# Performance work log

Measured on AMD Instinct MI355X. Metric: run time of the kernel, lower is better.

## Reference

```python
import jax, jax.numpy as jnp
import numpy as np

EPS = 1e-6


def _ln(x, gamma, beta):
    # torch LayerNorm variant here: uses unbiased std (ddof=1) and eps added to std
    mean = jnp.mean(x, axis=-1, keepdims=True)
    std = jnp.std(x, axis=-1, keepdims=True, ddof=1)
    return gamma * (x - mean) / (std + EPS) + beta


def setup_inputs() -> dict:
    key = jax.random.key(0)
    ks = jax.random.split(key, 5)
    B, In, H = 8192, 1024, 1024
    x = jax.random.normal(ks[0], (B, In), dtype=jnp.float32)
    h = jax.random.normal(ks[1], (B, H), dtype=jnp.float32)
    c = jax.random.normal(ks[2], (B, H), dtype=jnp.float32)
    w_ih = jax.random.normal(ks[3], (4 * H, In), dtype=jnp.float32) * (1.0 / np.sqrt(In))
    b_ih = jnp.zeros((4 * H,), dtype=jnp.float32)
    w_hh = jax.random.normal(ks[4], (4 * H, H), dtype=jnp.float32) * (1.0 / np.sqrt(H))
    gamma_ifgo = jnp.ones((4, H), dtype=jnp.float32)
    beta_ifgo = jnp.zeros((4, H), dtype=jnp.float32)
    gamma_c = jnp.ones((H,), dtype=jnp.float32)
    beta_c = jnp.zeros((H,), dtype=jnp.float32)
    return {"x": x, "h": h, "c": c, "w_ih": w_ih, "b_ih": b_ih, "w_hh": w_hh,
            "gamma_ifgo": gamma_ifgo, "beta_ifgo": beta_ifgo,
            "gamma_c": gamma_c, "beta_c": beta_c}


def reference(x, h, c, w_ih, b_ih, w_hh, gamma_ifgo, beta_ifgo, gamma_c, beta_c):
    B = x.shape[0]
    H = c.shape[1]
    # two GEMMs: [B,4H]
    v = jnp.einsum('bi,ki->bk', x, w_ih) + b_ih + jnp.einsum('bh,kh->bk', h, w_hh)
    gates = v.reshape(B, 4, H)  # stacked i, f, g, o (chunk order == stack order)
    gates = _ln(gates, gamma_ifgo, beta_ifgo)  # ParallelLayerNorm over last dim
    i, f, g, o = gates[:, 0], gates[:, 1], gates[:, 2], gates[:, 3]
    f = f + 1.0
    new_c = c * jax.nn.sigmoid(f) + jax.nn.sigmoid(i) * jnp.tanh(g)
    new_c = _ln(new_c, gamma_c, beta_c)
    new_h = jnp.tanh(new_c) * jax.nn.sigmoid(o)
    return new_h, new_c
```

## Files before the change

### kernel.cpp

```cpp
#include <hip/hip_runtime.h>
#include <hip/hip_bf16.h>
#include <cstdint>

typedef __bf16 bf16x8 __attribute__((ext_vector_type(8)));
typedef float  f32x4  __attribute__((ext_vector_type(4)));

#define BDIM 8192
#define KDIM 2048
#define NDIM 4096
#define HDIM 1024
#define LN_EPS 1e-6f
#define NT    (KDIM / 64)

__global__ __launch_bounds__(256) void cvt_concat_kernel(
    const float* __restrict__ p0, const float* __restrict__ p1,
    __bf16* __restrict__ dst, long total)
{
    long e = ((long)blockIdx.x * blockDim.x + threadIdx.x) * 8;
    if (e >= total) return;
    long row = e >> 11;
    long kk  = e & 2047;
    const float* src = (kk < 1024) ? (p0 + row * 1024 + kk)
                                   : (p1 + row * 1024 + (kk - 1024));
    float4 a = *(const float4*)(src);
    float4 b = *(const float4*)(src + 4);
    bf16x8 o;
    o[0] = (__bf16)a.x; o[1] = (__bf16)a.y; o[2] = (__bf16)a.z; o[3] = (__bf16)a.w;
    o[4] = (__bf16)b.x; o[5] = (__bf16)b.y; o[6] = (__bf16)b.z; o[7] = (__bf16)b.w;
    *(bf16x8*)(dst + e) = o;
}

__device__ inline void gload_lds16(const void* g, void* l) {
    __builtin_amdgcn_global_load_lds(
        (const __attribute__((address_space(1))) void*)g,
        (__attribute__((address_space(3))) void*)l, 16, 0, 0);
}

#define WAIT_VM(n) asm volatile("s_waitcnt vmcnt(" #n ")" ::: "memory")
#define BARRIER()  __builtin_amdgcn_s_barrier()

template<int Q>
__device__ inline void mma_q(f32x4 (&acc)[8][4],
                             const bf16x8 (&a)[2][2], const bf16x8 (&b)[4][2])
{
#pragma unroll
    for (int ks = 0; ks < 2; ++ks)
#pragma unroll
        for (int u = 0; u < 2; ++u)
#pragma unroll
            for (int nf = 0; nf < 4; ++nf)
                acc[2 * Q + u][nf] = __builtin_amdgcn_mfma_f32_16x16x32_bf16(
                    a[u][ks], b[nf][ks], acc[2 * Q + u][nf], 0, 0, 0);
}

__global__ __launch_bounds__(512, 2) void gemm_8phase_kernel(
    const __bf16* __restrict__ A, const __bf16* __restrict__ Bt,
    const float* __restrict__ bias, __bf16* __restrict__ V)
{
    __shared__ __bf16 smem[2][32768];

    const int tid = threadIdx.x;
    const int l   = tid & 63;
    const int w   = tid >> 6;
    const int wm  = w >> 2;
    const int wn  = w & 3;
    const int lane16 = l & 15;
    const int q16    = l >> 4;

    const int bid = blockIdx.x;
    const int swz = (bid & 7) * 64 + (bid >> 3);
    const int tileN = (swz & 15) * 256;
    const int tileM = (swz >> 4) * 256;

    const int srow  = (w >> 2) * 128 + (w & 3) * 8 + (l >> 3);
    const int sgran = (l & 7) ^ (l >> 3);
    const __bf16* Asrc = A  + (long)(tileM + srow) * KDIM + sgran * 8;
    const __bf16* Bsrc = Bt + (long)(tileN + srow) * KDIM + sgran * 8;
    const int a_dst = (w >> 2) * 8192 + (w & 3) * 512;
    const int b_dst = 16384 + a_dst;

    const int g0os = ((q16 ^ (l & 7))) * 8;
    const int g1os = (((q16 + 4) ^ (l & 7))) * 8;
    const int a_rd = wm * 8192 + lane16 * 64;
    const int b_rd = 16384 + wn * 4096 + lane16 * 64;

    f32x4 acc[8][4] = {};
    bf16x8 aX[2][2], aY[2][2], bP[4][2], bQ[4][2];

    auto stageA = [&](int c, int kt, int p) {
        gload_lds16(Asrc + (long)p * (32 * KDIM) + kt * 64, &smem[c][a_dst + p * 2048]);
    };
    auto stageB = [&](int c, int kt, int p) {
        gload_lds16(Bsrc + (long)p * (32 * KDIM) + kt * 64, &smem[c][b_dst + p * 2048]);
    };
    auto readA = [&](bf16x8 (&d)[2][2], int c, int q) {
        const __bf16* base = &smem[c][a_rd + q * 2048];
#pragma unroll
        for (int u = 0; u < 2; ++u) {
            d[u][0] = *(const bf16x8*)(base + u * 1024 + g0os);
            d[u][1] = *(const bf16x8*)(base + u * 1024 + g1os);
        }
    };
    auto readB = [&](bf16x8 (&d)[4][2], int c) {
        const __bf16* base = &smem[c][b_rd];
#pragma unroll
        for (int nf = 0; nf < 4; ++nf) {
            d[nf][0] = *(const bf16x8*)(base + nf * 1024 + g0os);
            d[nf][1] = *(const bf16x8*)(base + nf * 1024 + g1os);
        }
    };

#pragma unroll
    for (int p = 0; p < 4; ++p) { stageA(0, 0, p); stageB(0, 0, p); }
#pragma unroll
    for (int p = 0; p < 4; ++p) { stageA(1, 1, p); stageB(1, 1, p); }
    WAIT_VM(8);
    BARRIER();
    readB(bP, 0);
    readA(aX, 0, 0);
    asm volatile("s_waitcnt lgkmcnt(0)" ::: "memory");
    BARRIER();

#pragma unroll 1
    for (int i = 0; i < NT / 2; ++i) {
        const int k0 = 2 * i;
        const int k1 = 2 * i + 1;
        const bool st = (i < NT / 2 - 1);

        readA(aY, 0, 1);
        if (st) { stageA(0, k0 + 2, 0); stageB(0, k0 + 2, 0); }
        BARRIER();
        __builtin_amdgcn_s_setprio(1); mma_q<0>(acc, aX, bP); __builtin_amdgcn_s_setprio(0);

        readA(aX, 0, 2);
        if (st) { stageA(0, k0 + 2, 1); stageB(0, k0 + 2, 1); }
        BARRIER();
        __builtin_amdgcn_s_setprio(1); mma_q<1>(acc, aY, bP); __builtin_amdgcn_s_setprio(0);

        readA(aY, 0, 3);
        if (st) { stageA(0, k0 + 2, 2); stageB(0, k0 + 2, 2); }
        BARRIER();
        __builtin_amdgcn_s_setprio(1); mma_q<2>(acc, aX, bP); __builtin_amdgcn_s_setprio(0);

        if (st) { WAIT_VM(6); } else { WAIT_VM(0); }
        readB(bQ, 1);
        readA(aX, 1, 0);
        if (st) { stageA(0, k0 + 2, 3); stageB(0, k0 + 2, 3); }
        BARRIER();
        __builtin_amdgcn_s_setprio(1); mma_q<3>(acc, aY, bP); __builtin_amdgcn_s_setprio(0);

        readA(aY, 1, 1);
        if (st) { stageA(1, k1 + 2, 0); stageB(1, k1 + 2, 0); }
        BARRIER();
        __builtin_amdgcn_s_setprio(1); mma_q<0>(acc, aX, bQ); __builtin_amdgcn_s_setprio(0);

        readA(aX, 1, 2);
        if (st) { stageA(1, k1 + 2, 1); stageB(1, k1 + 2, 1); }
        BARRIER();
        __builtin_amdgcn_s_setprio(1); mma_q<1>(acc, aY, bQ); __builtin_amdgcn_s_setprio(0);

        readA(aY, 1, 3);
        if (st) { stageA(1, k1 + 2, 2); stageB(1, k1 + 2, 2); }
        BARRIER();
        __builtin_amdgcn_s_setprio(1); mma_q<2>(acc, aX, bQ); __builtin_amdgcn_s_setprio(0);

        if (st) {
            WAIT_VM(6);
            readB(bP, 0);
            readA(aX, 0, 0);
            stageA(1, k1 + 2, 3); stageB(1, k1 + 2, 3);
        }
        BARRIER();
        __builtin_amdgcn_s_setprio(1); mma_q<3>(acc, aY, bQ); __builtin_amdgcn_s_setprio(0);
    }

#pragma unroll
    for (int mi = 0; mi < 8; ++mi) {
        const int row = tileM + wm * 128 + mi * 16 + q16 * 4;
#pragma unroll
        for (int ni = 0; ni < 4; ++ni) {
            const int col = tileN + wn * 64 + ni * 16 + lane16;
            const float bv = bias[col];
#pragma unroll
            for (int j = 0; j < 4; ++j)
                V[(long)(row + j) * NDIM + col] = (__bf16)(acc[mi][ni][j] + bv);
        }
    }
}

__device__ inline float sigm_(float x) { return 1.f / (1.f + __expf(-x)); }
__device__ inline float tanh_(float x) { float e = __expf(2.f * x); return 1.f - 2.f / (e + 1.f); }

__global__ __launch_bounds__(256) void ln_lstm_kernel(
    const __bf16* __restrict__ v, const float* __restrict__ cin,
    const float* __restrict__ gamma4, const float* __restrict__ beta4,
    const float* __restrict__ gammac, const float* __restrict__ betac,
    float* __restrict__ out_h, float* __restrict__ out_c)
{
    __shared__ float gbuf[4][1024];
    __shared__ float red[8];

    const int b = blockIdx.x;
    const int t = threadIdx.x;
    const int w = t >> 6;
    const int l = t & 63;

    const __bf16* vb = v + (long)b * 4096 + w * 1024 + l * 16;
    bf16x8 v0 = *(const bf16x8*)(vb);
    bf16x8 v1 = *(const bf16x8*)(vb + 8);
    float xs[16];
#pragma unroll
    for (int q = 0; q < 8; ++q) { xs[q] = (float)v0[q]; xs[8 + q] = (float)v1[q]; }

    float s = 0.f, sq = 0.f;
#pragma unroll
    for (int q = 0; q < 16; ++q) { s += xs[q]; sq += xs[q] * xs[q]; }
#pragma unroll
    for (int m = 32; m >= 1; m >>= 1) { s += __shfl_xor(s, m); sq += __shfl_xor(sq, m); }

    const float mean = s * (1.f / 1024.f);
    const float var  = (sq - s * mean) * (1.f / 1023.f);
    const float invd = 1.f / (sqrtf(var) + LN_EPS);

#pragma unroll
    for (int q = 0; q < 16; ++q) {
        const int idx = l * 16 + q;
        gbuf[w][idx] = gamma4[w * 1024 + idx] * (xs[q] - mean) * invd + beta4[w * 1024 + idx];
    }
    __syncthreads();

    const int j0 = t * 4;
    float4 iv = *(const float4*)&gbuf[0][j0];
    float4 fv = *(const float4*)&gbuf[1][j0];
    float4 gv = *(const float4*)&gbuf[2][j0];
    float4 ov = *(const float4*)&gbuf[3][j0];
    float4 cv = *(const float4*)(cin + (long)b * 1024 + j0);

    float nc[4], oo[4];
    {
        const float ia[4] = {iv.x, iv.y, iv.z, iv.w};
        const float fa[4] = {fv.x, fv.y, fv.z, fv.w};
        const float ga[4] = {gv.x, gv.y, gv.z, gv.w};
        const float oa[4] = {ov.x, ov.y, ov.z, ov.w};
        const float ca[4] = {cv.x, cv.y, cv.z, cv.w};
#pragma unroll
        for (int q = 0; q < 4; ++q) {
            nc[q] = ca[q] * sigm_(fa[q] + 1.f) + sigm_(ia[q]) * tanh_(ga[q]);
            oo[q] = oa[q];
        }
    }

    float s2 = 0.f, sq2 = 0.f;
#pragma unroll
    for (int q = 0; q < 4; ++q) { s2 += nc[q]; sq2 += nc[q] * nc[q]; }
#pragma unroll
    for (int m = 32; m >= 1; m >>= 1) { s2 += __shfl_xor(s2, m); sq2 += __shfl_xor(sq2, m); }
    if (l == 0) { red[w] = s2; red[4 + w] = sq2; }
    __syncthreads();
    const float S  = red[0] + red[1] + red[2] + red[3];
    const float SQ = red[4] + red[5] + red[6] + red[7];
    const float mean2 = S * (1.f / 1024.f);
    const float var2  = (SQ - S * mean2) * (1.f / 1023.f);
    const float invd2 = 1.f / (sqrtf(var2) + LN_EPS);

    float4 hout, cout;
    float ho[4], co[4];
#pragma unroll
    for (int q = 0; q < 4; ++q) {
        const int j = j0 + q;
        const float ncl = gammac[j] * (nc[q] - mean2) * invd2 + betac[j];
        co[q] = ncl;
        ho[q] = tanh_(ncl) * sigm_(oo[q]);
    }
    hout.x = ho[0]; hout.y = ho[1]; hout.z = ho[2]; hout.w = ho[3];
    cout.x = co[0]; cout.y = co[1]; cout.z = co[2]; cout.w = co[3];
    *(float4*)(out_h + (long)b * 1024 + j0) = hout;
    *(float4*)(out_c + (long)b * 1024 + j0) = cout;
}

extern "C" void kernel_launch(void* const* d_in, const int* in_sizes, int n_in,
                              void* d_out, int out_size, void* d_ws, size_t ws_size,
                              hipStream_t stream)
{
    const float* x      = (const float*)d_in[0];
    const float* h      = (const float*)d_in[1];
    const float* c      = (const float*)d_in[2];
    const float* w_ih   = (const float*)d_in[3];
    const float* b_ih   = (const float*)d_in[4];
    const float* w_hh   = (const float*)d_in[5];
    const float* gamma4 = (const float*)d_in[6];
    const float* beta4  = (const float*)d_in[7];
    const float* gammac = (const float*)d_in[8];
    const float* betac  = (const float*)d_in[9];

    char* ws = (char*)d_ws;
    const size_t szA = (size_t)BDIM * KDIM * 2;
    const size_t szB = (size_t)NDIM * KDIM * 2;
    const size_t szV = (size_t)BDIM * NDIM * 2;
    if (ws_size < szA + szB + szV) return;

    __bf16* Abf = (__bf16*)ws;
    __bf16* Bbf = (__bf16*)(ws + szA);
    __bf16* v   = (__bf16*)(ws + szA + szB);

    float* out_h = (float*)d_out;
    float* out_c = out_h + (size_t)BDIM * HDIM;

    {
        long totA = (long)BDIM * KDIM;
        long totB = (long)NDIM * KDIM;
        cvt_concat_kernel<<<dim3((unsigned)(totA / 8 / 256)), dim3(256), 0, stream>>>(x, h, Abf, totA);
        cvt_concat_kernel<<<dim3((unsigned)(totB / 8 / 256)), dim3(256), 0, stream>>>(w_ih, w_hh, Bbf, totB);
    }

    gemm_8phase_kernel<<<dim3((BDIM / 256) * (NDIM / 256)), dim3(512), 0, stream>>>(
        Abf, Bbf, b_ih, v);

    ln_lstm_kernel<<<dim3(BDIM), dim3(256), 0, stream>>>(
        v, c, gamma4, beta4, gammac, betac, out_h, out_c);
}
```

Before: 200.7 us.

## Make GEMM blocks handle two M tiles sequentially and merge conversion kernels

New measurement: 207.4 us. 3.3% more time.

```diff
diff --git a/kernel.cpp b/kernel.cpp
--- a/kernel.cpp
+++ b/kernel.cpp
@@ -10,16 +10,22 @@
 #define NDIM 4096
 #define HDIM 1024
 #define LN_EPS 1e-6f
-#define NT    (KDIM / 64)
-
-__global__ __launch_bounds__(256) void cvt_concat_kernel(
-    const float* __restrict__ p0, const float* __restrict__ p1,
-    __bf16* __restrict__ dst, long total)
+#define NKT   64
+#define NITER (NKT / 2)
+#define TOTA  ((long)BDIM * KDIM)
+#define TOTB  ((long)NDIM * KDIM)
+
+__global__ __launch_bounds__(256) void cvt_all_kernel(
+    const float* __restrict__ x, const float* __restrict__ h,
+    const float* __restrict__ wih, const float* __restrict__ whh,
+    __bf16* __restrict__ Abf, __bf16* __restrict__ Bbf)
 {
     long e = ((long)blockIdx.x * blockDim.x + threadIdx.x) * 8;
-    if (e >= total) return;
-    long row = e >> 11;
-    long kk  = e & 2047;
+    const float* p0; const float* p1; __bf16* dst; long eo;
+    if (e < TOTA) { p0 = x;   p1 = h;   dst = Abf; eo = e; }
+    else          { p0 = wih; p1 = whh; dst = Bbf; eo = e - TOTA; }
+    long row = eo >> 11;
+    long kk  = eo & 2047;
     const float* src = (kk < 1024) ? (p0 + row * 1024 + kk)
                                    : (p1 + row * 1024 + (kk - 1024));
     float4 a = *(const float4*)(src);
@@ -27,7 +33,7 @@
     bf16x8 o;
     o[0] = (__bf16)a.x; o[1] = (__bf16)a.y; o[2] = (__bf16)a.z; o[3] = (__bf16)a.w;
     o[4] = (__bf16)b.x; o[5] = (__bf16)b.y; o[6] = (__bf16)b.z; o[7] = (__bf16)b.w;
-    *(bf16x8*)(dst + e) = o;
+    *(bf16x8*)(dst + eo) = o;
 }
 
 __device__ inline void gload_lds16(const void* g, void* l) {
@@ -68,9 +74,9 @@
     const int q16    = l >> 4;
 
     const int bid = blockIdx.x;
-    const int swz = (bid & 7) * 64 + (bid >> 3);
+    const int swz = (bid & 7) * 32 + (bid >> 3);
     const int tileN = (swz & 15) * 256;
-    const int tileM = (swz >> 4) * 256;
+    const int tileM = (swz >> 4) * 512;
 
     const int srow  = (w >> 2) * 128 + (w & 3) * 8 + (l >> 3);
     const int sgran = (l & 7) ^ (l >> 3);
@@ -88,10 +94,12 @@
     bf16x8 aX[2][2], aY[2][2], bP[4][2], bQ[4][2];
 
     auto stageA = [&](int c, int kt, int p) {
-        gload_lds16(Asrc + (long)p * (32 * KDIM) + kt * 64, &smem[c][a_dst + p * 2048]);
+        const long off = (long)(kt >> 5) * (256L * KDIM) + (long)(kt & 31) * 64;
+        gload_lds16(Asrc + off + (long)p * (32 * KDIM), &smem[c][a_dst + p * 2048]);
     };
     auto stageB = [&](int c, int kt, int p) {
-        gload_lds16(Bsrc + (long)p * (32 * KDIM) + kt * 64, &smem[c][b_dst + p * 2048]);
+        gload_lds16(Bsrc + (long)(kt & 31) * 64 + (long)p * (32 * KDIM),
+                    &smem[c][b_dst + p * 2048]);
     };
     auto readA = [&](bf16x8 (&d)[2][2], int c, int q) {
         const __bf16* base = &smem[c][a_rd + q * 2048];
@@ -107,6 +115,20 @@
         for (int nf = 0; nf < 4; ++nf) {
             d[nf][0] = *(const bf16x8*)(base + nf * 1024 + g0os);
             d[nf][1] = *(const bf16x8*)(base + nf * 1024 + g1os);
+        }
+    };
+    auto writeC = [&](int rowbase) {
+#pragma unroll
+        for (int mi = 0; mi < 8; ++mi) {
+            const int row = rowbase + wm * 128 + mi * 16 + q16 * 4;
+#pragma unroll
+            for (int ni = 0; ni < 4; ++ni) {
+                const int col = tileN + wn * 64 + ni * 16 + lane16;
+                const float bv = bias[col];
+#pragma unroll
+                for (int j = 0; j < 4; ++j)
+                    V[(long)(row + j) * NDIM + col] = (__bf16)(acc[mi][ni][j] + bv);
+            }
         }
     };
 
@@ -122,10 +144,19 @@
     BARRIER();
 
 #pragma unroll 1
-    for (int i = 0; i < NT / 2; ++i) {
+    for (int i = 0; i < NITER; ++i) {
+        if (i == NITER / 2) {
+            writeC(tileM);
+#pragma unroll
+            for (int mi = 0; mi < 8; ++mi)
+#pragma unroll
+                for (int ni = 0; ni < 4; ++ni)
+                    acc[mi][ni] = (f32x4){0.f, 0.f, 0.f, 0.f};
+        }
+
         const int k0 = 2 * i;
         const int k1 = 2 * i + 1;
-        const bool st = (i < NT / 2 - 1);
+        const bool st = (i < NITER - 1);
 
         readA(aY, 0, 1);
         if (st) { stageA(0, k0 + 2, 0); stageB(0, k0 + 2, 0); }
@@ -174,18 +205,7 @@
         __builtin_amdgcn_s_setprio(1); mma_q<3>(acc, aY, bQ); __builtin_amdgcn_s_setprio(0);
     }
 
-#pragma unroll
-    for (int mi = 0; mi < 8; ++mi) {
-        const int row = tileM + wm * 128 + mi * 16 + q16 * 4;
-#pragma unroll
-        for (int ni = 0; ni < 4; ++ni) {
-            const int col = tileN + wn * 64 + ni * 16 + lane16;
-            const float bv = bias[col];
-#pragma unroll
-            for (int j = 0; j < 4; ++j)
-                V[(long)(row + j) * NDIM + col] = (__bf16)(acc[mi][ni][j] + bv);
-        }
-    }
+    writeC(tileM + 256);
 }
 
 __device__ inline float sigm_(float x) { return 1.f / (1.f + __expf(-x)); }
@@ -306,15 +326,10 @@
     float* out_h = (float*)d_out;
     float* out_c = out_h + (size_t)BDIM * HDIM;
 
-    {
-        long totA = (long)BDIM * KDIM;
-        long totB = (long)NDIM * KDIM;
-        cvt_concat_kernel<<<dim3((unsigned)(totA / 8 / 256)), dim3(256), 0, stream>>>(x, h, Abf, totA);
-        cvt_concat_kernel<<<dim3((unsigned)(totB / 8 / 256)), dim3(256), 0, stream>>>(w_ih, w_hh, Bbf, totB);
-    }
-
-    gemm_8phase_kernel<<<dim3((BDIM / 256) * (NDIM / 256)), dim3(512), 0, stream>>>(
-        Abf, Bbf, b_ih, v);
+    cvt_all_kernel<<<dim3((unsigned)((TOTA + TOTB) / 8 / 256)), dim3(256), 0, stream>>>(
+        x, h, w_ih, w_hh, Abf, Bbf);
+
+    gemm_8phase_kernel<<<dim3(256), dim3(512), 0, stream>>>(Abf, Bbf, b_ih, v);
 
     ln_lstm_kernel<<<dim3(BDIM), dim3(256), 0, stream>>>(
         v, c, gamma4, beta4, gammac, betac, out_h, out_c);
```
